# Performance work log

Measured on AMD Instinct MI355X. Metric: run time of the kernel, lower is better.

The kernel has to match this reference:

```python
import jax, jax.numpy as jnp
import numpy as np

HEADS = 8
D_MODEL = 512
HEAD_DIM = D_MODEL // HEADS


def setup_inputs() -> dict:
    key = jax.random.key(0)
    ks = jax.random.split(key, 13)
    B, S, D = 8, 1024, D_MODEL
    scale = 1.0 / np.sqrt(D)
    x = jax.random.normal(ks[0], (B, S, D), dtype=jnp.float32)
    names = ['cq', 'ck', 'cv', 'pq', 'pk', 'pv']
    inp = {'x': x}
    for i, n in enumerate(names):
        inp['W_' + n] = jax.random.normal(ks[1 + 2 * i], (D, D), dtype=jnp.float32) * scale
        inp['b_' + n] = jax.random.normal(ks[2 + 2 * i], (D,), dtype=jnp.float32) * 0.01
    return inp


def reference(x, W_cq, b_cq, W_ck, b_ck, W_cv, b_cv, W_pq, b_pq, W_pk, b_pk, W_pv, b_pv):
    # x: [N, S, D]. Fused common + personal QKV: (x@Wc + bc) + (x@Wp + bp)
    N, S, D = x.shape
    q = x @ (W_cq + W_pq) + (b_cq + b_pq)  # [N, S, D]
    k = x @ (W_ck + W_pk) + (b_ck + b_pk)
    v = x @ (W_cv + W_pv) + (b_cv + b_pv)
    q = q.reshape(N, S, HEADS, HEAD_DIM)
    k = k.reshape(N, S, HEADS, HEAD_DIM)
    v = v.reshape(N, S, HEADS, HEAD_DIM)
    # NOTE: original scales by sqrt(d_model), not sqrt(head_dim)
    energy = jnp.einsum('nqhd,nkhd->nhqk', q, k) / jnp.sqrt(jnp.asarray(D, x.dtype))
    attn = jax.nn.softmax(energy, axis=-1)  # [N, H, Q, K]
    out = jnp.einsum('nhqk,nkhd->nqhd', attn, v).reshape(N, S, D)
    return out
```

## Files before the change

kernel.cpp:

```cpp
#include <hip/hip_runtime.h>

#define B_   8
#define S_   1024
#define D_   512
#define H_   8
#define HD_  64
#define NT_  (B_ * S_)
#define QSCALE_ 0.06376387f
#define C4_    5.7707802f

typedef _Float16 f16;
typedef _Float16 f16x2 __attribute__((ext_vector_type(2)));
typedef _Float16 f16x4 __attribute__((ext_vector_type(4)));
typedef _Float16 f16x8 __attribute__((ext_vector_type(8)));
typedef float    f32x4 __attribute__((ext_vector_type(4)));

#define GLOAD_LDS16(g, l) \
    __builtin_amdgcn_global_load_lds( \
        (const __attribute__((address_space(1))) unsigned int*)(g), \
        (__attribute__((address_space(3))) unsigned int*)(l), 16, 0, 0)

#define MFMA16(a, b, c) __builtin_amdgcn_mfma_f32_16x16x32_f16(a, b, c, 0, 0, 0)

#define CVT_PK(p0, p1) __builtin_bit_cast(f16x2, __builtin_amdgcn_cvt_pkrtz(p0, p1))


__global__ __launch_bounds__(256) void prep_fused(
    const float* __restrict__ x, f16* __restrict__ xh_t,
    const float* __restrict__ Wcq, const float* __restrict__ Wck, const float* __restrict__ Wcv,
    const float* __restrict__ Wpq, const float* __restrict__ Wpk, const float* __restrict__ Wpv,
    f16* __restrict__ Bt_t)
{
    __shared__ float tile[64][68];
    const int tid = threadIdx.x;

    if (blockIdx.x < 1024) {
        const int mtile = blockIdx.x >> 4;
        const int ktile = blockIdx.x & 15;
        f16* dst = xh_t + ((size_t)mtile * 16 + ktile) * 4096;
#pragma unroll
        for (int half = 0; half < 2; ++half) {
            const int q = half * 256 + tid;
            const int r = q >> 2;
            const int c = q & 3;
            const float* src = x + (size_t)(mtile * 128 + r) * D_ + ktile * 32 + c * 8;
            float4 a = *(const float4*)(src);
            float4 b = *(const float4*)(src + 4);
            f16x8 o = { (f16)a.x, (f16)a.y, (f16)a.z, (f16)a.w,
                        (f16)b.x, (f16)b.y, (f16)b.z, (f16)b.w };
            *(f16x8*)(dst + c * 1024 + r * 8) = o;
        }
        return;
    }

    const int wk = blockIdx.x - 1024;
    const int k0 = (wk & 7) * 64;
    const int n0 = (wk >> 3) * 64;
    const int g  = n0 >> 9;
    const int c0 = n0 & 511;
    const float* Wc = (g == 0) ? Wcq : (g == 1) ? Wck : Wcv;
    const float* Wp = (g == 0) ? Wpq : (g == 1) ? Wpk : Wpv;

#pragma unroll
    for (int it = 0; it < 4; ++it) {
        int row = it * 16 + (tid >> 4);
        int c4  = (tid & 15) * 4;
        float4 a = *(const float4*)(Wc + (size_t)(k0 + row) * D_ + c0 + c4);
        float4 b = *(const float4*)(Wp + (size_t)(k0 + row) * D_ + c0 + c4);
        tile[row][c4 + 0] = a.x + b.x;
        tile[row][c4 + 1] = a.y + b.y;
        tile[row][c4 + 2] = a.z + b.z;
        tile[row][c4 + 3] = a.w + b.w;
    }
    __syncthreads();

    const int ntile = n0 >> 7;
    const int rbase = n0 & 64;
#pragma unroll
    for (int it = 0; it < 2; ++it) {
        int nr = it * 32 + (tid >> 3);
        int kc = (tid & 7) * 8;
        f16x8 o;
#pragma unroll
        for (int j = 0; j < 8; ++j) o[j] = (f16)tile[kc + j][nr];
        const int kt = (k0 + kc) >> 5;
        const int c  = (kc >> 3) & 3;
        const int r  = rbase + nr;
        *(f16x8*)(Bt_t + ((size_t)ntile * 16 + kt) * 4096 + c * 1024 + r * 8) = o;
    }
}

__global__ __launch_bounds__(256) void qkv_gemm(
    const f16* __restrict__ xh_t, const f16* __restrict__ Bt_t,
    const float* __restrict__ bcq, const float* __restrict__ bck, const float* __restrict__ bcv,
    const float* __restrict__ bpq, const float* __restrict__ bpk, const float* __restrict__ bpv,
    f16* __restrict__ Qh, f16* __restrict__ Kws, f16* __restrict__ Vws)
{
    __shared__ __align__(16) char smem_raw[36864];

    const int bid   = blockIdx.x;
    const int xcd   = bid & 7;
    const int idx   = bid >> 3;
    const int mtile = xcd * 8 + (idx & 7);
    const int ntile = idx >> 3;
    const int m0 = mtile * 128;
    const int n0 = ntile * 128;

    const int tid  = threadIdx.x;
    const int lane = tid & 63;
    const int wave = tid >> 6;
    const int wr = wave >> 1, wc = wave & 1;
    const int lo4 = lane & 15, hi4 = lane >> 4;

    const f16* gA = xh_t + (size_t)mtile * 16 * 4096;
    const f16* gB = Bt_t + (size_t)ntile * 16 * 4096;

#define STAGE(bufsel, kt) do { \
        f16* _A = (f16*)(smem_raw + (bufsel) * 16384); \
        f16* _B = (f16*)(smem_raw + (bufsel) * 16384 + 8192); \
        GLOAD_LDS16(gA + (kt) * 4096 + tid * 8,         _A + tid * 8);         \
        GLOAD_LDS16(gA + (kt) * 4096 + (tid + 256) * 8, _A + (tid + 256) * 8); \
        GLOAD_LDS16(gB + (kt) * 4096 + tid * 8,         _B + tid * 8);         \
        GLOAD_LDS16(gB + (kt) * 4096 + (tid + 256) * 8, _B + (tid + 256) * 8); \
    } while (0)

    f32x4 acc[4][4];
#pragma unroll
    for (int i = 0; i < 4; ++i)
#pragma unroll
        for (int j = 0; j < 4; ++j) acc[i][j] = (f32x4){0.f, 0.f, 0.f, 0.f};

    STAGE(0, 0);
    asm volatile("s_waitcnt vmcnt(0)" ::: "memory");
    __syncthreads();

    for (int t = 0; t < 16; ++t) {
        const int cur = t & 1;
        if (t < 15) STAGE(cur ^ 1, t + 1);

        const f16* Ab = (const f16*)(smem_raw + cur * 16384);
        const f16* Bb = (const f16*)(smem_raw + cur * 16384 + 8192);
        f16x8 a[4], b[4];
#pragma unroll
        for (int i = 0; i < 4; ++i)
            a[i] = *(const f16x8*)(Ab + hi4 * 1024 + (wr * 64 + i * 16 + lo4) * 8);
#pragma unroll
        for (int j = 0; j < 4; ++j)
            b[j] = *(const f16x8*)(Bb + hi4 * 1024 + (wc * 64 + j * 16 + lo4) * 8);
#pragma unroll
        for (int i = 0; i < 4; ++i)
#pragma unroll
            for (int j = 0; j < 4; ++j)
                acc[i][j] = MFMA16(a[i], b[j], acc[i][j]);

        asm volatile("s_waitcnt vmcnt(0)" ::: "memory");
        __syncthreads();
    }
#undef STAGE

    const int g = n0 >> 9;
    const float* bc = (g == 0) ? bcq : (g == 1) ? bck : bcv;
    const float* bp = (g == 0) ? bpq : (g == 1) ? bpk : bpv;

    const int colb = n0 + wc * 64;
    const int h    = (colb & 511) >> 6;
    const int rowb = m0 + wr * 64;
    const int bb   = rowb >> 10;
    const int s0   = rowb & 1023;

    float bias[4];
#pragma unroll
    for (int j = 0; j < 4; ++j) {
        const int cg = (colb + j * 16 + lo4) & 511;
        bias[j] = bc[cg] + bp[cg];
    }

    f16* Cs = (f16*)smem_raw + wave * 4608;
    const size_t bhbase = (size_t)(bb * H_ + h) * 65536;

    if (g == 2) {
#pragma unroll
        for (int i = 0; i < 4; ++i)
#pragma unroll
            for (int j = 0; j < 4; ++j) {
                f16x4 v = { (f16)(acc[i][j][0] + bias[j]), (f16)(acc[i][j][1] + bias[j]),
                            (f16)(acc[i][j][2] + bias[j]), (f16)(acc[i][j][3] + bias[j]) };
                *(f16x4*)(Cs + (j * 16 + lo4) * 72 + i * 16 + hi4 * 4) = v;
            }
        asm volatile("s_waitcnt lgkmcnt(0)" ::: "memory");
        __builtin_amdgcn_sched_barrier(0);
        const size_t tbase = bhbase + (size_t)(s0 >> 6) * 4096;
#pragma unroll
        for (int it = 0; it < 8; ++it) {
            const int d  = it * 8 + (lane >> 3);
            const int cs = lane & 7;
            f16x8 chunk = *(const f16x8*)(Cs + d * 72 + cs * 8);
            *(f16x8*)(Vws + tbase + d * 64 + ((cs ^ (d & 7)) << 3)) = chunk;
        }
    } else {
        const float scale = (g == 0) ? QSCALE_ : 1.f;
#pragma unroll
        for (int i = 0; i < 4; ++i)
#pragma unroll
            for (int j = 0; j < 4; ++j)
#pragma unroll
                for (int r = 0; r < 4; ++r)
                    Cs[(i * 16 + hi4 * 4 + r) * 72 + j * 16 + lo4] =
                        (f16)((acc[i][j][r] + bias[j]) * scale);
        asm volatile("s_waitcnt lgkmcnt(0)" ::: "memory");
        __builtin_amdgcn_sched_barrier(0);
#pragma unroll
        for (int it = 0; it < 8; ++it) {
            const int rr = it * 8 + (lane >> 3);
            const int ci = lane & 7;
            f16x8 chunk = *(const f16x8*)(Cs + rr * 72 + ci * 8);
            if (g == 0) {
                *(f16x8*)(Qh + bhbase + (size_t)(s0 + rr) * 64 + ci * 8) = chunk;
            } else {
                const size_t tbase = bhbase + (size_t)(s0 >> 6) * 4096;
                *(f16x8*)(Kws + tbase + rr * 64 + ((ci ^ (rr & 7)) << 3)) = chunk;
            }
        }
    }
}

__global__ __launch_bounds__(256) void attn_fwd(
    const f16* __restrict__ Qh, const f16* __restrict__ Kws,
    const f16* __restrict__ Vws, float* __restrict__ out)
{
    __shared__ __align__(16) f16 Ks[2][4096];
    __shared__ __align__(16) f16 Vs[2][4096];
    __shared__ __align__(16) f16 Ps[4][32 * 72];
    __shared__ float Lw[4][32];

    const int b0 = blockIdx.x;
    const int bh = (b0 & 7) * 8 + ((b0 >> 3) & 7);
    const int qt = b0 >> 6;

    const int wave = threadIdx.x >> 6;
    const int lane = threadIdx.x & 63;
    const int lo4 = lane & 15, hi4 = lane >> 4;
    const int q0 = qt * 128 + wave * 32;

    const f16* Qp = Qh  + (size_t)bh * 65536;
    const f16* Kp = Kws + (size_t)bh * 65536;
    const f16* Vp = Vws + (size_t)bh * 65536;
    f16* Pw = &Ps[wave][0];

    f16x8 aq[2][2];
#pragma unroll
    for (int qg = 0; qg < 2; ++qg)
#pragma unroll
        for (int hh = 0; hh < 2; ++hh)
            aq[qg][hh] = *(const f16x8*)(Qp + (q0 + qg * 16 + lo4) * 64 + hh * 32 + hi4 * 8);

    f32x4 o[2][4];
    float l[2] = {0.f, 0.f};
#pragma unroll
    for (int qg = 0; qg < 2; ++qg)
#pragma unroll
        for (int dt = 0; dt < 4; ++dt)
            o[qg][dt] = (f32x4){0.f, 0.f, 0.f, 0.f};

    const int soff = threadIdx.x * 8;

    {
        f16x8 ka = *(const f16x8*)(Kp + soff);
        f16x8 kb = *(const f16x8*)(Kp + 2048 + soff);
        f16x8 va = *(const f16x8*)(Vp + soff);
        f16x8 vb = *(const f16x8*)(Vp + 2048 + soff);
        *(f16x8*)(&Ks[0][soff])        = ka;
        *(f16x8*)(&Ks[0][2048 + soff]) = kb;
        *(f16x8*)(&Vs[0][soff])        = va;
        *(f16x8*)(&Vs[0][2048 + soff]) = vb;
    }
    __syncthreads();

    for (int t = 0; t < 16; ++t) {
        const int cur = t & 1;

        f16x8 kna, knb, vna, vnb;
        if (t < 15) {
            const f16* Kn = Kp + (t + 1) * 4096;
            const f16* Vn = Vp + (t + 1) * 4096;
            kna = *(const f16x8*)(Kn + soff);
            knb = *(const f16x8*)(Kn + 2048 + soff);
            vna = *(const f16x8*)(Vn + soff);
            vnb = *(const f16x8*)(Vn + 2048 + soff);
        }

        const f16* Kc = &Ks[cur][0];
        const f16* Vc = &Vs[cur][0];

#pragma unroll
        for (int f = 0; f < 4; ++f) {
            const int c = f * 16 + lo4;
            f16x8 bk0 = *(const f16x8*)(Kc + c * 64 + ((hi4 ^ (c & 7)) << 3));
            f16x8 bk1 = *(const f16x8*)(Kc + c * 64 + (((4 + hi4) ^ (c & 7)) << 3));
#pragma unroll
            for (int qg = 0; qg < 2; ++qg) {
                f32x4 sc = (f32x4){0.f, 0.f, 0.f, 0.f};
                sc = MFMA16(bk0, aq[qg][0], sc);
                sc = MFMA16(bk1, aq[qg][1], sc);
                float p0 = __builtin_amdgcn_exp2f(sc[0] - C4_);
                float p1 = __builtin_amdgcn_exp2f(sc[1] - C4_);
                float p2 = __builtin_amdgcn_exp2f(sc[2] - C4_);
                float p3 = __builtin_amdgcn_exp2f(sc[3] - C4_);
                l[qg] += (p0 + p1) + (p2 + p3);
                f16x2 a01 = CVT_PK(p0, p1);
                f16x2 a23 = CVT_PK(p2, p3);
                f16x4 pv = { a01[0], a01[1], a23[0], a23[1] };
                *(f16x4*)(Pw + (qg * 16 + lo4) * 72 + f * 16 + hi4 * 4) = pv;
            }
        }
        asm volatile("s_waitcnt lgkmcnt(0)" ::: "memory");
        __builtin_amdgcn_sched_barrier(0);

        f16x8 ap[2][2];
#pragma unroll
        for (int qg = 0; qg < 2; ++qg) {
            ap[qg][0] = *(const f16x8*)(Pw + (qg * 16 + lo4) * 72 + hi4 * 8);
            ap[qg][1] = *(const f16x8*)(Pw + (qg * 16 + lo4) * 72 + 32 + hi4 * 8);
        }
#pragma unroll
        for (int dt = 0; dt < 4; ++dt) {
            const int d = dt * 16 + lo4;
            f16x8 bv0 = *(const f16x8*)(Vc + d * 64 + ((hi4 ^ (d & 7)) << 3));
            f16x8 bv1 = *(const f16x8*)(Vc + d * 64 + (((4 + hi4) ^ (d & 7)) << 3));
#pragma unroll
            for (int qg = 0; qg < 2; ++qg) {
                o[qg][dt] = MFMA16(ap[qg][0], bv0, o[qg][dt]);
                o[qg][dt] = MFMA16(ap[qg][1], bv1, o[qg][dt]);
            }
        }

        if (t < 15) {
            *(f16x8*)(&Ks[cur ^ 1][soff])        = kna;
            *(f16x8*)(&Ks[cur ^ 1][2048 + soff]) = knb;
            *(f16x8*)(&Vs[cur ^ 1][soff])        = vna;
            *(f16x8*)(&Vs[cur ^ 1][2048 + soff]) = vnb;
        }
        __syncthreads();
    }

#pragma unroll
    for (int qg = 0; qg < 2; ++qg) {
        l[qg] += __shfl_xor(l[qg], 16);
        l[qg] += __shfl_xor(l[qg], 32);
    }
    if (lane < 16) {
        Lw[wave][lane]      = l[0];
        Lw[wave][16 + lane] = l[1];
    }
    asm volatile("s_waitcnt lgkmcnt(0)" ::: "memory");
    __builtin_amdgcn_sched_barrier(0);

    const int b = bh >> 3;
    const int h = bh & 7;
#pragma unroll
    for (int qg = 0; qg < 2; ++qg)
#pragma unroll
        for (int r = 0; r < 4; ++r) {
            const float inv = 1.f / Lw[wave][qg * 16 + hi4 * 4 + r];
            const int s_idx = q0 + qg * 16 + hi4 * 4 + r;
            float* op = out + ((size_t)(b * S_ + s_idx)) * D_ + h * HD_;
#pragma unroll
            for (int dt = 0; dt < 4; ++dt)
                op[dt * 16 + lo4] = o[qg][dt][r] * inv;
        }
}

extern "C" void kernel_launch(void* const* d_in, const int* in_sizes, int n_in,
                              void* d_out, int out_size, void* d_ws, size_t ws_size,
                              hipStream_t stream)
{
    const float* x   = (const float*)d_in[0];
    const float* Wcq = (const float*)d_in[1];
    const float* bcq = (const float*)d_in[2];
    const float* Wck = (const float*)d_in[3];
    const float* bck = (const float*)d_in[4];
    const float* Wcv = (const float*)d_in[5];
    const float* bcv = (const float*)d_in[6];
    const float* Wpq = (const float*)d_in[7];
    const float* bpq = (const float*)d_in[8];
    const float* Wpk = (const float*)d_in[9];
    const float* bpk = (const float*)d_in[10];
    const float* Wpv = (const float*)d_in[11];
    const float* bpv = (const float*)d_in[12];

    f16* ws = (f16*)d_ws;
    f16* xh_t = ws;
    f16* Bt_t = xh_t + (size_t)64 * 16 * 4096;
    f16* Qh   = Bt_t + (size_t)12 * 16 * 4096;
    f16* Kws  = Qh + (size_t)64 * 65536;
    f16* Vws  = Kws + (size_t)64 * 65536;
    float* o = (float*)d_out;

    prep_fused<<<1216, 256, 0, stream>>>(x, xh_t, Wcq, Wck, Wcv, Wpq, Wpk, Wpv, Bt_t);
    qkv_gemm<<<768, 256, 0, stream>>>(xh_t, Bt_t, bcq, bck, bcv, bpq, bpk, bpv,
                                      Qh, Kws, Vws);
    attn_fwd<<<512, 256, 0, stream>>>(Qh, Kws, Vws, o);
}
```

Before: 53.91 us.

## Software-pipeline attention loop: overlap PV of previous tile with QK of current

Restructures the attention main loop so each iteration first runs the P·V MFMAs for the previous K/V tile and then computes QK scores and exp for the current tile. P is double-buffered in LDS and V becomes triple-buffered, so the intra-wave lgkmcnt wait between writing P and reading it back is replaced by the block barrier. The aim is to hide the LDS round-trip and exp latency behind independent MFMA work. In exchange it uses more shared memory, which may lower occupancy, and adds a separate epilogue for the last tile.

```diff
diff --git a/kernel.cpp b/kernel.cpp
--- a/kernel.cpp
+++ b/kernel.cpp
@@ -229,8 +229,8 @@
     const f16* __restrict__ Vws, float* __restrict__ out)
 {
     __shared__ __align__(16) f16 Ks[2][4096];
-    __shared__ __align__(16) f16 Vs[2][4096];
-    __shared__ __align__(16) f16 Ps[4][32 * 72];
+    __shared__ __align__(16) f16 Vs[3][4096];
+    __shared__ __align__(16) f16 Ps[2][4][32 * 72];
     __shared__ float Lw[4][32];
 
     const int b0 = blockIdx.x;
@@ -245,7 +245,6 @@
     const f16* Qp = Qh  + (size_t)bh * 65536;
     const f16* Kp = Kws + (size_t)bh * 65536;
     const f16* Vp = Vws + (size_t)bh * 65536;
-    f16* Pw = &Ps[wave][0];
 
     f16x8 aq[2][2];
 #pragma unroll
@@ -276,9 +275,9 @@
     }
     __syncthreads();
 
+    int vprev = 2, vcur = 0, vnext = 1;
+
     for (int t = 0; t < 16; ++t) {
-        const int cur = t & 1;
-
         f16x8 kna, knb, vna, vnb;
         if (t < 15) {
             const f16* Kn = Kp + (t + 1) * 4096;
@@ -289,38 +288,73 @@
             vnb = *(const f16x8*)(Vn + 2048 + soff);
         }
 
-        const f16* Kc = &Ks[cur][0];
-        const f16* Vc = &Vs[cur][0];
-
-#pragma unroll
-        for (int f = 0; f < 4; ++f) {
-            const int c = f * 16 + lo4;
-            f16x8 bk0 = *(const f16x8*)(Kc + c * 64 + ((hi4 ^ (c & 7)) << 3));
-            f16x8 bk1 = *(const f16x8*)(Kc + c * 64 + (((4 + hi4) ^ (c & 7)) << 3));
+        if (t > 0) {
+            const f16* Pr = &Ps[(t - 1) & 1][wave][0];
+            const f16* Vc = &Vs[vprev][0];
+            f16x8 ap[2][2];
 #pragma unroll
             for (int qg = 0; qg < 2; ++qg) {
-                f32x4 sc = (f32x4){0.f, 0.f, 0.f, 0.f};
-                sc = MFMA16(bk0, aq[qg][0], sc);
-                sc = MFMA16(bk1, aq[qg][1], sc);
-                float p0 = __builtin_amdgcn_exp2f(sc[0] - C4_);
-                float p1 = __builtin_amdgcn_exp2f(sc[1] - C4_);
-                float p2 = __builtin_amdgcn_exp2f(sc[2] - C4_);
-                float p3 = __builtin_amdgcn_exp2f(sc[3] - C4_);
-                l[qg] += (p0 + p1) + (p2 + p3);
-                f16x2 a01 = CVT_PK(p0, p1);
-                f16x2 a23 = CVT_PK(p2, p3);
-                f16x4 pv = { a01[0], a01[1], a23[0], a23[1] };
-                *(f16x4*)(Pw + (qg * 16 + lo4) * 72 + f * 16 + hi4 * 4) = pv;
-            }
-        }
-        asm volatile("s_waitcnt lgkmcnt(0)" ::: "memory");
-        __builtin_amdgcn_sched_barrier(0);
-
+                ap[qg][0] = *(const f16x8*)(Pr + (qg * 16 + lo4) * 72 + hi4 * 8);
+                ap[qg][1] = *(const f16x8*)(Pr + (qg * 16 + lo4) * 72 + 32 + hi4 * 8);
+            }
+#pragma unroll
+            for (int dt = 0; dt < 4; ++dt) {
+                const int d = dt * 16 + lo4;
+                f16x8 bv0 = *(const f16x8*)(Vc + d * 64 + ((hi4 ^ (d & 7)) << 3));
+                f16x8 bv1 = *(const f16x8*)(Vc + d * 64 + (((4 + hi4) ^ (d & 7)) << 3));
+#pragma unroll
+                for (int qg = 0; qg < 2; ++qg) {
+                    o[qg][dt] = MFMA16(ap[qg][0], bv0, o[qg][dt]);
+                    o[qg][dt] = MFMA16(ap[qg][1], bv1, o[qg][dt]);
+                }
+            }
+        }
+
+        {
+            const f16* Kc = &Ks[t & 1][0];
+            f16* Pw = &Ps[t & 1][wave][0];
+#pragma unroll
+            for (int f = 0; f < 4; ++f) {
+                const int c = f * 16 + lo4;
+                f16x8 bk0 = *(const f16x8*)(Kc + c * 64 + ((hi4 ^ (c & 7)) << 3));
+                f16x8 bk1 = *(const f16x8*)(Kc + c * 64 + (((4 + hi4) ^ (c & 7)) << 3));
+#pragma unroll
+                for (int qg = 0; qg < 2; ++qg) {
+                    f32x4 sc = (f32x4){0.f, 0.f, 0.f, 0.f};
+                    sc = MFMA16(bk0, aq[qg][0], sc);
+                    sc = MFMA16(bk1, aq[qg][1], sc);
+                    float p0 = __builtin_amdgcn_exp2f(sc[0] - C4_);
+                    float p1 = __builtin_amdgcn_exp2f(sc[1] - C4_);
+                    float p2 = __builtin_amdgcn_exp2f(sc[2] - C4_);
+                    float p3 = __builtin_amdgcn_exp2f(sc[3] - C4_);
+                    l[qg] += (p0 + p1) + (p2 + p3);
+                    f16x2 a01 = CVT_PK(p0, p1);
+                    f16x2 a23 = CVT_PK(p2, p3);
+                    f16x4 pv = { a01[0], a01[1], a23[0], a23[1] };
+                    *(f16x4*)(Pw + (qg * 16 + lo4) * 72 + f * 16 + hi4 * 4) = pv;
+                }
+            }
+        }
+
+        if (t < 15) {
+            *(f16x8*)(&Ks[(t + 1) & 1][soff])        = kna;
+            *(f16x8*)(&Ks[(t + 1) & 1][2048 + soff]) = knb;
+            *(f16x8*)(&Vs[vnext][soff])              = vna;
+            *(f16x8*)(&Vs[vnext][2048 + soff])       = vnb;
+        }
+        __syncthreads();
+
+        vprev = vcur; vcur = vnext; vnext = (vnext == 2) ? 0 : vnext + 1;
+    }
+
+    {
+        const f16* Pr = &Ps[1][wave][0];
+        const f16* Vc = &Vs[vprev][0];
         f16x8 ap[2][2];
 #pragma unroll
         for (int qg = 0; qg < 2; ++qg) {
-            ap[qg][0] = *(const f16x8*)(Pw + (qg * 16 + lo4) * 72 + hi4 * 8);
-            ap[qg][1] = *(const f16x8*)(Pw + (qg * 16 + lo4) * 72 + 32 + hi4 * 8);
+            ap[qg][0] = *(const f16x8*)(Pr + (qg * 16 + lo4) * 72 + hi4 * 8);
+            ap[qg][1] = *(const f16x8*)(Pr + (qg * 16 + lo4) * 72 + 32 + hi4 * 8);
         }
 #pragma unroll
         for (int dt = 0; dt < 4; ++dt) {
@@ -333,14 +367,6 @@
                 o[qg][dt] = MFMA16(ap[qg][1], bv1, o[qg][dt]);
             }
         }
-
-        if (t < 15) {
-            *(f16x8*)(&Ks[cur ^ 1][soff])        = kna;
-            *(f16x8*)(&Ks[cur ^ 1][2048 + soff]) = knb;
-            *(f16x8*)(&Vs[cur ^ 1][soff])        = vna;
-            *(f16x8*)(&Vs[cur ^ 1][2048 + soff]) = vnb;
-        }
-        __syncthreads();
     }
 
 #pragma unroll
```

New measurement: 56.57 us. 4.9% more time.
